# Kernel tuning notes

Hardware: AMD Instinct MI355X
Metric: run time of the kernel (lower is better)

## Reference

```python
import jax, jax.numpy as jnp
import numpy as np

L = 16            # clip_len
STRIDES = (2, 2)
RADII = (0.15, 0.3)
NSAMPLES = (16, 32)
EPS = 1e-5
NEG_SLOPE = 0.2


def _fps(xyz, npoint):
    # furthest point sampling, xyz: (N, 3) -> (npoint,) int32 indices, start at 0
    N = xyz.shape[0]
    def step(carry, _):
        mind, last = carry
        d = jnp.sum((xyz - xyz[last]) ** 2, axis=-1)
        mind = jnp.minimum(mind, d)
        nxt = jnp.argmax(mind).astype(jnp.int32)
        return (mind, nxt), nxt
    _, rest = jax.lax.scan(step, (jnp.full((N,), 1e10, xyz.dtype), jnp.int32(0)), None, length=npoint - 1)
    return jnp.concatenate([jnp.zeros((1,), jnp.int32), rest])


def _shift_point(xyz, batch, N):
    # torch.roll(points, -1, dims=1) over the temporal axis, with last-frame extrapolation fix
    p = xyz.reshape(batch // L, L, N, 3)
    s = jnp.roll(p, -1, axis=1)
    shift_mean = jnp.mean(s[:, :-1] - p[:, :-1], axis=1)   # (Bc, N, 3)
    s = s.at[:, -1].set(p[:, -1] + shift_mean)
    return s.reshape(batch, N, 3)


def _conv_bn_lrelu(x, w, g, b):
    # 1x1 Conv2d (no bias) + GroupBN (per-channel over all other dims) + LeakyReLU(0.2)
    y = jnp.einsum('oc,bcnk->bonk', w, x)
    mu = jnp.mean(y, axis=(0, 2, 3), keepdims=True)
    var = jnp.var(y, axis=(0, 2, 3), keepdims=True)
    y = (y - mu) * jax.lax.rsqrt(var + EPS) * g[None, :, None, None] + b[None, :, None, None]
    return jnp.where(y > 0, y, NEG_SLOPE * y)


def _sa_module(xyz, features, stride, radius, nsample, layers):
    # xyz: (B, N, 3), features: (B, C, N)
    batch, N = xyz.shape[0], xyz.shape[1]
    q = _shift_point(xyz, batch, N)
    npoint = N // stride if stride > 1 else N
    if stride > 1:
        idx = jax.vmap(lambda p: _fps(p, npoint))(jax.lax.stop_gradient(q))  # (B, npoint)
        q = jax.vmap(lambda p, ix: p[ix])(q, idx)                            # (B, npoint, 3)
    # ball query: first `nsample` neighbors of each query within `radius`, padded with first hit
    d2 = jnp.sum((q[:, :, None, :] - xyz[:, None, :, :]) ** 2, axis=-1)      # (B, npoint, N)
    mask = d2 < radius * radius
    cand = jnp.where(mask, jnp.arange(N, dtype=jnp.int32)[None, None, :], N)
    srt = jnp.sort(cand, axis=-1)[..., :nsample]
    first = srt[..., :1]
    gidx = jnp.where(srt == N, first, srt)
    gidx = jnp.where(gidx == N, 0, gidx)                                     # fallback: no neighbor
    grouped_xyz = jax.vmap(lambda pts, ix: pts[ix])(xyz, gidx)               # (B, npoint, ns, 3)
    dp = (grouped_xyz - q[:, :, None, :]) / radius                           # normalize_dp
    dist = jnp.linalg.norm(dp, axis=-1)                                      # (B, npoint, ns) -> 4th grouped channel
    feats = jnp.swapaxes(features, 1, 2)                                     # (B, N, C)
    grouped_f = jax.vmap(lambda f, ix: f[ix])(feats, gidx)                   # (B, npoint, ns, C)
    x = jnp.concatenate([dp, grouped_f], axis=-1)                            # (B, npoint, ns, 3 + C)
    x = jnp.transpose(x, (0, 3, 1, 2))                                       # (B, 3 + C, npoint, ns)
    for (w, g, b) in layers:
        x = _conv_bn_lrelu(x, w, g, b)
    gate = jax.nn.sigmoid(dist)[:, None, :, :]                               # sigmoid(points[:, -1:])
    out = jnp.max(gate * x, axis=-1)                                         # (B, Cout, npoint)
    return q, out


def _forward(xyz, w1a, g1a, b1a, w1b, g1b, b1b, w2a, g2a, b2a, w2b, g2b, b2b):
    features = jnp.swapaxes(xyz, 1, 2)                                       # features default = xyz^T
    q1, f1 = _sa_module(xyz, features, STRIDES[0], RADII[0], NSAMPLES[0],
                        [(w1a, g1a, b1a), (w1b, g1b, b1b)])
    q2, f2 = _sa_module(q1, f1, STRIDES[1], RADII[1], NSAMPLES[1],
                        [(w2a, g2a, b2a), (w2b, g2b, b2b)])
    return f2                                                                # (32, 256, 128)


def setup_inputs() -> dict:
    key = jax.random.key(0)
    ks = jax.random.split(key, 5)
    B, N = 32, 512   # B = 2 clips * clip_len 16
    xyz = jax.random.uniform(ks[0], (B, N, 3), jnp.float32)
    def w(k, o, i):
        return jax.random.normal(k, (o, i), jnp.float32) / np.sqrt(i).astype(np.float32)
    return {
        'xyz': xyz,
        'w1a': w(ks[1], 64, 6),    'g1a': jnp.ones(64),  'b1a': jnp.zeros(64),
        'w1b': w(ks[2], 128, 64),  'g1b': jnp.ones(128), 'b1b': jnp.zeros(128),
        'w2a': w(ks[3], 128, 131), 'g2a': jnp.ones(128), 'b2a': jnp.zeros(128),
        'w2b': w(ks[4], 256, 128), 'g2b': jnp.ones(256), 'b2b': jnp.zeros(256),
    }


def reference(xyz, w1a, g1a, b1a, w1b, g1b, b1b, w2a, g2a, b2a, w2b, g2b, b2b):
    return _forward(xyz, w1a, g1a, b1a, w1b, g1b, b1b, w2a, g2a, b2a, w2b, g2b, b2b)
```

## Files before the change

### kernel.cpp

```cpp
#include <hip/hip_runtime.h>
#include <hip/hip_bf16.h>
#include <math.h>


#define BATCH 32
#define MCOLS 131072
#define CGRID 2048

typedef __attribute__((ext_vector_type(8))) short short8;
typedef __attribute__((ext_vector_type(4))) short short4v;
typedef __attribute__((ext_vector_type(4))) float f32x4;

__device__ __forceinline__ float b2f(short s) {
    return __uint_as_float(((unsigned)(unsigned short)s) << 16);
}
__device__ __forceinline__ short f2b(float f) {
    __hip_bfloat16 h = __float2bfloat16(f);
    return (short)__builtin_bit_cast(unsigned short, h);
}
__device__ __forceinline__ float dpp_row16_sum(float v) {
    int x;
    x = __builtin_amdgcn_update_dpp(0, __float_as_int(v), 0x111, 0xf, 0xf, true);
    v += __int_as_float(x);
    x = __builtin_amdgcn_update_dpp(0, __float_as_int(v), 0x112, 0xf, 0xf, true);
    v += __int_as_float(x);
    x = __builtin_amdgcn_update_dpp(0, __float_as_int(v), 0x114, 0xf, 0xf, true);
    v += __int_as_float(x);
    x = __builtin_amdgcn_update_dpp(0, __float_as_int(v), 0x118, 0xf, 0xf, true);
    v += __int_as_float(x);
    return v;
}
template<int C>
__device__ __forceinline__ float dpp_max(float v) {
    int x = __builtin_amdgcn_update_dpp(0, __float_as_int(v), C, 0xf, 0xf, true);
    return fmaxf(v, __int_as_float(x));
}
__device__ __forceinline__ float readlane_f(float v, int lane) {
    return __int_as_float(__builtin_amdgcn_readlane(__float_as_int(v), lane));
}

__global__ void prep_w(const float* __restrict__ w, int O, int C, int CK,
                       short* __restrict__ hi, short* __restrict__ lo) {
    int t = blockIdx.x * 256 + threadIdx.x;
    if (t >= O * CK) return;
    int o = t / CK, c = t % CK;
    float f = (c < C) ? w[o * C + c] : 0.f;
    short h = f2b(f);
    float fh = b2f(h);
    int NT = O >> 4;
    int ot = o >> 4, l15 = o & 15;
    int kc = c >> 5, quad = (c & 31) >> 3, j = c & 7;
    size_t idx = (((size_t)kc * NT + ot) * 64 + quad * 16 + l15) * 8 + j;
    hi[idx] = h;
    lo[idx] = f2b(f - fh);
}

template<int N>
__global__ void shift_kernel(const float* __restrict__ xyz, float* __restrict__ qout) {
    int t = blockIdx.x * 256 + threadIdx.x;
    if (t >= BATCH * N * 3) return;
    int c = t % 3;
    int n = (t / 3) % N;
    int b = t / (3 * N);
    int l = b & 15;
    float v;
    if (l < 15) {
        v = xyz[((size_t)(b + 1) * N + n) * 3 + c];
    } else {
        int g0 = b - 15;
        float acc = 0.f;
        for (int i = 0; i < 15; ++i) {
            float d = __fsub_rn(xyz[((size_t)(g0 + i + 1) * N + n) * 3 + c],
                                xyz[((size_t)(g0 + i) * N + n) * 3 + c]);
            acc = __fadd_rn(acc, d);
        }
        v = __fadd_rn(xyz[((size_t)b * N + n) * 3 + c], __fdiv_rn(acc, 15.f));
    }
    qout[t] = v;
}

template<int N, int NPOINT>
__global__ __launch_bounds__(64) void fps_kernel(const float* __restrict__ q,
                                                 float* __restrict__ qsel) {
    int b = blockIdx.x;
    int lane = threadIdx.x;
    constexpr int P = N / 64;
    __shared__ float4 qp[N];
    __shared__ int sel[NPOINT];
    const float* qb = q + (size_t)b * N * 3;
    for (int j = lane; j < N; j += 64)
        qp[j] = make_float4(qb[j * 3 + 0], qb[j * 3 + 1], qb[j * 3 + 2], 0.f);
    if (lane == 0) sel[0] = 0;
    __syncthreads();
    float px[P], py[P], pz[P], mind[P];
#pragma unroll
    for (int p = 0; p < P; ++p) {
        float4 v = qp[lane * P + p];
        px[p] = v.x; py[p] = v.y; pz[p] = v.z;
        mind[p] = 1e10f;
    }
    float4 L0 = qp[0];
    float lx = L0.x, ly = L0.y, lz = L0.z;
    for (int s = 1; s < NPOINT; ++s) {
        float bestd = -1.f;
        int bestp = 0;
        float bx = 0.f, by = 0.f, bz = 0.f;
#pragma unroll
        for (int p = 0; p < P; ++p) {
            float dx = __fsub_rn(px[p], lx);
            float dy = __fsub_rn(py[p], ly);
            float dz = __fsub_rn(pz[p], lz);
            float d = __fadd_rn(__fadd_rn(__fmul_rn(dx, dx), __fmul_rn(dy, dy)),
                                __fmul_rn(dz, dz));
            float mn = fminf(mind[p], d);
            mind[p] = mn;
            bool g = mn > bestd;
            bestd = g ? mn : bestd;
            bestp = g ? p : bestp;
            bx = g ? px[p] : bx;
            by = g ? py[p] : by;
            bz = g ? pz[p] : bz;
        }
        float m = bestd;
        m = dpp_max<0x111>(m);
        m = dpp_max<0x112>(m);
        m = dpp_max<0x114>(m);
        m = dpp_max<0x118>(m);
        m = dpp_max<0x142>(m);
        m = dpp_max<0x143>(m);
        float maxd = readlane_f(m, 63);
        unsigned long long msk = __ballot(bestd == maxd);
        int winner = (int)__builtin_ctzll(msk);
        int wp = __builtin_amdgcn_readlane(bestp, winner);
        int last = winner * P + wp;
        lx = readlane_f(bx, winner);
        ly = readlane_f(by, winner);
        lz = readlane_f(bz, winner);
        if (lane == 0) sel[s] = last;
    }
    __syncthreads();
    for (int i = lane; i < NPOINT; i += 64) {
        float4 Pt = qp[sel[i]];
        size_t o = ((size_t)b * NPOINT + i) * 3;
        qsel[o + 0] = Pt.x;
        qsel[o + 1] = Pt.y;
        qsel[o + 2] = Pt.z;
    }
}

template<int N, int NPOINT, int NS, int CF, int CK>
__global__ __launch_bounds__(256) void ballq_kernel(
        const float* __restrict__ xyz,
        const float* __restrict__ qpts,
        const float* __restrict__ feats,
        float r2, float radius,
        short* __restrict__ X, float* __restrict__ gate) {
    static_assert((NS & (NS - 1)) == 0, "NS pow2");
    int lane = threadIdx.x & 63;
    int wib = threadIdx.x >> 6;
    int wid = blockIdx.x * 4 + wib;
    int b = wid / NPOINT;
    int i = wid % NPOINT;
    const float* qp = qpts + ((size_t)b * NPOINT + i) * 3;
    float qx = qp[0], qy = qp[1], qz = qp[2];
    __shared__ int gsh[4][NS];
    int* gidx = gsh[wib];
    int taken = 0, first = 0;
    bool any = false;
#pragma unroll
    for (int base = 0; base < N; base += 64) {
        int j = base + lane;
        const float* p = xyz + ((size_t)b * N + j) * 3;
        float dx = __fsub_rn(qx, p[0]);
        float dy = __fsub_rn(qy, p[1]);
        float dz = __fsub_rn(qz, p[2]);
        float d2 = __fadd_rn(__fadd_rn(__fmul_rn(dx, dx), __fmul_rn(dy, dy)),
                             __fmul_rn(dz, dz));
        bool in = d2 < r2;
        unsigned long long mk = __ballot(in);
        if (!any && mk) { first = base + __builtin_ctzll(mk); any = true; }
        int cb = __builtin_popcountll(mk & ((1ull << lane) - 1ull));
        int slot = taken + cb;
        if (in && slot < NS) gidx[slot] = j;
        taken += (int)__builtin_popcountll(mk);
    }
    if (taken < NS) {
        for (int s = taken + lane; s < NS; s += 64) gidx[s] = any ? first : 0;
    }
    __syncthreads();
    int m0 = (b * NPOINT + i) * NS;
    if (lane < NS) {
        int g = gidx[lane];
        const float* p = xyz + ((size_t)b * N + g) * 3;
        float dx = (p[0] - qx) / radius;
        float dy = (p[1] - qy) / radius;
        float dz = (p[2] - qz) / radius;
        float dist = sqrtf(dx * dx + dy * dy + dz * dz);
        gate[m0 + lane] = 1.f / (1.f + expf(-dist));
    }
    for (int e = lane; e < NS * CK; e += 64) {
        int s = e / CK;
        int c = e % CK;
        int g = gidx[s];
        float v;
        if (c < 3) {
            float qc = (c == 0) ? qx : ((c == 1) ? qy : qz);
            v = (xyz[((size_t)b * N + g) * 3 + c] - qc) / radius;
        } else if (c < 3 + CF) {
            v = feats[((size_t)b * N + g) * CF + (c - 3)];
        } else {
            v = 0.f;
        }
        X[(size_t)(m0 + s) * CK + c] = f2b(v);
    }
}

template<int CK, int O, bool AFF>
__global__ __launch_bounds__(256, 3) void mfma_conv(
        const short* __restrict__ X, const short* __restrict__ Whi,
        const short* __restrict__ Wlo, const float* __restrict__ ss,
        short* __restrict__ Y, float* __restrict__ pS, float* __restrict__ pS2) {
    constexpr int KC = CK / 32;
    constexpr int NT = O / 16;
    constexpr int OW = NT / 4;
    constexpr int LR = CK + 8;
    constexpr int CB = CK / 8;
    __shared__ __align__(16) short xs[64 * LR];
    __shared__ __align__(16) short wh[NT * 512];
    __shared__ __align__(16) short wl[NT * 512];
    __shared__ float ssl[AFF ? 2 * CK : 1];
    __shared__ float sblk[O], s2blk[O];
    int tid = threadIdx.x;
    int m0 = blockIdx.x * 64;

    if constexpr (AFF) {
        for (int i = tid; i < 2 * CK; i += 256) ssl[i] = ss[i];
        __syncthreads();
    }
    for (int idx = tid; idx < 64 * CB; idx += 256) {
        int r = idx / CB;
        int col = (idx % CB) * 8;
        short8 v = *(const short8*)(X + (size_t)(m0 + r) * CK + col);
        if constexpr (AFF) {
#pragma unroll
            for (int i = 0; i < 8; ++i) {
                float f = b2f(v[i]);
                f = fmaf(f, ssl[col + i], ssl[CK + col + i]);
                f = f > 0.f ? f : 0.2f * f;
                v[i] = f2b(f);
            }
        }
        *(short8*)(xs + r * LR + col) = v;
    }

    int lane = tid & 63;
    int wave = tid >> 6;
    int l15 = lane & 15;
    int quad = lane >> 4;
    int obase = wave * OW * 16;

    f32x4 acc[4][OW];
#pragma unroll
    for (int mt = 0; mt < 4; ++mt)
#pragma unroll
        for (int ot = 0; ot < OW; ++ot) acc[mt][ot] = (f32x4){0.f, 0.f, 0.f, 0.f};

    for (int kc = 0; kc < KC; ++kc) {
        __syncthreads();
        {
            const short8* gH = (const short8*)Whi + (size_t)kc * NT * 64;
            const short8* gL = (const short8*)Wlo + (size_t)kc * NT * 64;
            short8* lH = (short8*)wh;
            short8* lL = (short8*)wl;
            for (int i = tid; i < NT * 64; i += 256) { lH[i] = gH[i]; lL[i] = gL[i]; }
        }
        __syncthreads();
        short8 bf[4];
#pragma unroll
        for (int mt = 0; mt < 4; ++mt)
            bf[mt] = *(const short8*)(xs + (mt * 16 + l15) * LR + kc * 32 + quad * 8);
#pragma unroll
        for (int ot = 0; ot < OW; ++ot) {
            short8 ah = ((const short8*)wh)[(wave * OW + ot) * 64 + lane];
            short8 al = ((const short8*)wl)[(wave * OW + ot) * 64 + lane];
#pragma unroll
            for (int mt = 0; mt < 4; ++mt) {
                acc[mt][ot] = __builtin_amdgcn_mfma_f32_16x16x32_bf16(ah, bf[mt], acc[mt][ot], 0, 0, 0);
                acc[mt][ot] = __builtin_amdgcn_mfma_f32_16x16x32_bf16(al, bf[mt], acc[mt][ot], 0, 0, 0);
            }
        }
    }

#pragma unroll
    for (int mt = 0; mt < 4; ++mt) {
        size_t ybase = (size_t)(m0 + mt * 16 + l15) * O + obase + quad * 4;
#pragma unroll
        for (int ot = 0; ot < OW; ++ot) {
            short4v pk;
#pragma unroll
            for (int r4 = 0; r4 < 4; ++r4) pk[r4] = f2b(acc[mt][ot][r4]);
            *(short4v*)(Y + ybase + ot * 16) = pk;
        }
    }
#pragma unroll
    for (int ot = 0; ot < OW; ++ot) {
#pragma unroll
        for (int r4 = 0; r4 < 4; ++r4) {
            float s = 0.f, s2 = 0.f;
#pragma unroll
            for (int mt = 0; mt < 4; ++mt) {
                float v = acc[mt][ot][r4];
                s += v;
                s2 = fmaf(v, v, s2);
            }
            s = dpp_row16_sum(s);
            s2 = dpp_row16_sum(s2);
            if (l15 == 15) {
                int o = obase + ot * 16 + quad * 4 + r4;
                sblk[o] = s;
                s2blk[o] = s2;
            }
        }
    }
    __syncthreads();
    for (int o = tid; o < O; o += 256) {
        pS [(size_t)o * CGRID + blockIdx.x] = sblk[o];
        pS2[(size_t)o * CGRID + blockIdx.x] = s2blk[o];
    }
}

template<int O>
__global__ __launch_bounds__(256) void stats_fin(
        const float* __restrict__ pS, const float* __restrict__ pS2,
        const float* __restrict__ gm, const float* __restrict__ bt,
        float* __restrict__ norm) {
    int o = blockIdx.x;
    float s = 0.f, s2 = 0.f;
    for (int p = threadIdx.x; p < CGRID; p += 256) {
        s += pS[(size_t)o * CGRID + p];
        s2 += pS2[(size_t)o * CGRID + p];
    }
#pragma unroll
    for (int off = 32; off >= 1; off >>= 1) {
        s  += __shfl_xor(s,  off, 64);
        s2 += __shfl_xor(s2, off, 64);
    }
    __shared__ float sh[8];
    int wid = threadIdx.x >> 6;
    if ((threadIdx.x & 63) == 0) { sh[wid] = s; sh[4 + wid] = s2; }
    __syncthreads();
    if (threadIdx.x == 0) {
        float S  = sh[0] + sh[1] + sh[2] + sh[3];
        float S2 = sh[4] + sh[5] + sh[6] + sh[7];
        const float invM = 1.f / (float)MCOLS;
        float mu = S * invM;
        float var = S2 * invM - mu * mu;
        float sc = gm[o] * rsqrtf(var + 1e-5f);
        norm[o] = sc;
        norm[O + o] = bt[o] - mu * sc;
    }
}

template<int NS, int NPOINT, int O>
__global__ __launch_bounds__(256) void pool1_kernel(
        const short* __restrict__ Y, const float* __restrict__ norm,
        const float* __restrict__ gate, float* __restrict__ out) {
    int t = blockIdx.x * 256 + threadIdx.x;
    int o = t % O;
    int n = (t / O) % NPOINT;
    int b = t / (O * NPOINT);
    int m0 = (b * NPOINT + n) * NS;
    float sc = norm[o], sf = norm[O + o];
    float best = -INFINITY;
#pragma unroll
    for (int k = 0; k < NS; ++k) {
        float v = fmaf(b2f(Y[(size_t)(m0 + k) * O + o]), sc, sf);
        v = v > 0.f ? v : 0.2f * v;
        best = fmaxf(best, gate[m0 + k] * v);
    }
    out[t] = best;
}

__global__ __launch_bounds__(256) void pool2_kernel(
        const short* __restrict__ Y, const float* __restrict__ norm,
        const float* __restrict__ gate, float* __restrict__ out) {
    constexpr int NS = 32, NPOINT = 128, O = 256;
    int b  = blockIdx.x >> 3;
    int oc = (blockIdx.x >> 1) & 3;
    int nc = blockIdx.x & 1;
    __shared__ float trans[64][65];
    int tid = threadIdx.x;
    for (int w = 0; w < 16; ++w) {
        int idx = w * 256 + tid;
        int o_l = idx & 63;
        int n_l = idx >> 6;
        int o = oc * 64 + o_l;
        int n = nc * 64 + n_l;
        int m0 = (b * NPOINT + n) * NS;
        float sc = norm[o], sf = norm[O + o];
        float best = -INFINITY;
#pragma unroll
        for (int k = 0; k < NS; ++k) {
            float v = fmaf(b2f(Y[(size_t)(m0 + k) * O + o]), sc, sf);
            v = v > 0.f ? v : 0.2f * v;
            best = fmaxf(best, gate[m0 + k] * v);
        }
        trans[o_l][n_l] = best;
    }
    __syncthreads();
    for (int w = 0; w < 16; ++w) {
        int idx = w * 256 + tid;
        int o_l = idx >> 6;
        int n_l = idx & 63;
        out[((size_t)b * O + oc * 64 + o_l) * NPOINT + nc * 64 + n_l] = trans[o_l][n_l];
    }
}

extern "C" void kernel_launch(void* const* d_in, const int* in_sizes, int n_in,
                              void* d_out, int out_size, void* d_ws, size_t ws_size,
                              hipStream_t stream) {
    const float* xyz = (const float*)d_in[0];
    const float* w1a = (const float*)d_in[1];
    const float* g1a = (const float*)d_in[2];
    const float* b1a = (const float*)d_in[3];
    const float* w1b = (const float*)d_in[4];
    const float* g1b = (const float*)d_in[5];
    const float* b1b = (const float*)d_in[6];
    const float* w2a = (const float*)d_in[7];
    const float* g2a = (const float*)d_in[8];
    const float* b2a = (const float*)d_in[9];
    const float* w2b = (const float*)d_in[10];
    const float* g2b = (const float*)d_in[11];
    const float* b2b = (const float*)d_in[12];

    char* ws = (char*)d_ws;
    constexpr size_t OFF_Q1C   = 0;
    constexpr size_t OFF_GATE1 = 98304;
    constexpr size_t OFF_Q2C   = 622592;
    constexpr size_t OFF_GATE2 = 671744;
    constexpr size_t OFF_NORM  = 1196032;
    constexpr size_t OFF_W     = 1204224;
    constexpr size_t OFF_PS    = 1499136;
    constexpr size_t OFF_PS2   = 3596288;
    constexpr size_t OFF_A     = 5693440;
    constexpr size_t OFF_B     = 39247872;
    constexpr size_t OFF_F1    = OFF_B + 41943040;

    float* q1c   = (float*)(ws + OFF_Q1C);
    float* gate1 = (float*)(ws + OFF_GATE1);
    float* q2c   = (float*)(ws + OFF_Q2C);
    float* gate2 = (float*)(ws + OFF_GATE2);
    float* n1a   = (float*)(ws + OFF_NORM);
    float* n1b   = (float*)(ws + OFF_NORM + 512);
    float* n2a   = (float*)(ws + OFF_NORM + 1536);
    float* n2b   = (float*)(ws + OFF_NORM + 2560);
    short* w1aH  = (short*)(ws + OFF_W);
    short* w1aL  = w1aH + 2048;
    short* w1bH  = w1aL + 2048;
    short* w1bL  = w1bH + 8192;
    short* w2aH  = w1bL + 8192;
    short* w2aL  = w2aH + 20480;
    short* w2bH  = w2aL + 20480;
    short* w2bL  = w2bH + 32768;
    float* pS    = (float*)(ws + OFF_PS);
    float* pS2   = (float*)(ws + OFF_PS2);

    char* A = ws + OFF_A;
    char* B = ws + OFF_B;
    short* X1  = (short*)A;
    short* Y1a = (short*)B;
    short* Y1b = (short*)A;
    short* X2  = (short*)B;
    short* Y2a = (short*)A;
    short* Y2b = (short*)B;
    float* qs1 = (float*)B;
    float* qs2 = (float*)A;
    float* f1  = (float*)(ws + OFF_F1);

    const float r2_1 = (float)(0.15 * 0.15);
    const float r2_2 = (float)(0.3 * 0.3);

    prep_w<<<8,   256, 0, stream>>>(w1a, 64, 6, 32, w1aH, w1aL);
    prep_w<<<32,  256, 0, stream>>>(w1b, 128, 64, 64, w1bH, w1bL);
    prep_w<<<80,  256, 0, stream>>>(w2a, 128, 131, 160, w2aH, w2aL);
    prep_w<<<128, 256, 0, stream>>>(w2b, 256, 128, 128, w2bH, w2bL);

    shift_kernel<512><<<192, 256, 0, stream>>>(xyz, qs1);
    fps_kernel<512, 256><<<32, 64, 0, stream>>>(qs1, q1c);
    ballq_kernel<512, 256, 16, 3, 32><<<2048, 256, 0, stream>>>(
        xyz, q1c, xyz, r2_1, 0.15f, X1, gate1);
    mfma_conv<32, 64, false><<<CGRID, 256, 0, stream>>>(X1, w1aH, w1aL, nullptr, Y1a, pS, pS2);
    stats_fin<64><<<64, 256, 0, stream>>>(pS, pS2, g1a, b1a, n1a);
    mfma_conv<64, 128, true><<<CGRID, 256, 0, stream>>>(Y1a, w1bH, w1bL, n1a, Y1b, pS, pS2);
    stats_fin<128><<<128, 256, 0, stream>>>(pS, pS2, g1b, b1b, n1b);
    pool1_kernel<16, 256, 128><<<4096, 256, 0, stream>>>(Y1b, n1b, gate1, f1);

    shift_kernel<256><<<96, 256, 0, stream>>>(q1c, qs2);
    fps_kernel<256, 128><<<32, 64, 0, stream>>>(qs2, q2c);
    ballq_kernel<256, 128, 32, 128, 160><<<1024, 256, 0, stream>>>(
        q1c, q2c, f1, r2_2, 0.3f, X2, gate2);
    mfma_conv<160, 128, false><<<CGRID, 256, 0, stream>>>(X2, w2aH, w2aL, nullptr, Y2a, pS, pS2);
    stats_fin<128><<<128, 256, 0, stream>>>(pS, pS2, g2a, b2a, n2a);
    mfma_conv<128, 256, true><<<CGRID, 256, 0, stream>>>(Y2a, w2bH, w2bL, n2a, Y2b, pS, pS2);
    stats_fin<256><<<256, 256, 0, stream>>>(pS, pS2, g2b, b2b, n2b);
    pool2_kernel<<<256, 256, 0, stream>>>(Y2b, n2b, gate2, (float*)d_out);
}
```

Before: 409.5 us.

## Fuse temporal shift into FPS kernel and use tree-max selection in FPS loop

Removes the separate shift_kernel launches and computes the rolled/extrapolated coordinates while loading points into shared memory inside fps_kernel. The per-thread argmax in the FPS loop becomes a tree fmax reduction followed by an equality scan to recover index and coordinates, which shortens the serial dependency chain on each of the sequential FPS iterations. The goal is to save two launches and the round trip of the shifted coordinates through global memory, and to cut latency in the FPS loop that bounds this pipeline. The cost is that the block handling frame 15 now does the 15-frame mean loads itself, serially within one 64-thread block.

```diff
diff --git a/kernel.cpp b/kernel.cpp
--- a/kernel.cpp
+++ b/kernel.cpp
@@ -55,41 +55,36 @@
     lo[idx] = f2b(f - fh);
 }
 
-template<int N>
-__global__ void shift_kernel(const float* __restrict__ xyz, float* __restrict__ qout) {
-    int t = blockIdx.x * 256 + threadIdx.x;
-    if (t >= BATCH * N * 3) return;
-    int c = t % 3;
-    int n = (t / 3) % N;
-    int b = t / (3 * N);
-    int l = b & 15;
-    float v;
-    if (l < 15) {
-        v = xyz[((size_t)(b + 1) * N + n) * 3 + c];
-    } else {
-        int g0 = b - 15;
-        float acc = 0.f;
-        for (int i = 0; i < 15; ++i) {
-            float d = __fsub_rn(xyz[((size_t)(g0 + i + 1) * N + n) * 3 + c],
-                                xyz[((size_t)(g0 + i) * N + n) * 3 + c]);
-            acc = __fadd_rn(acc, d);
-        }
-        v = __fadd_rn(xyz[((size_t)b * N + n) * 3 + c], __fdiv_rn(acc, 15.f));
-    }
-    qout[t] = v;
-}
-
 template<int N, int NPOINT>
-__global__ __launch_bounds__(64) void fps_kernel(const float* __restrict__ q,
+__global__ __launch_bounds__(64) void fps_kernel(const float* __restrict__ src,
                                                  float* __restrict__ qsel) {
     int b = blockIdx.x;
     int lane = threadIdx.x;
+    int l = b & 15;
     constexpr int P = N / 64;
     __shared__ float4 qp[N];
     __shared__ int sel[NPOINT];
-    const float* qb = q + (size_t)b * N * 3;
-    for (int j = lane; j < N; j += 64)
-        qp[j] = make_float4(qb[j * 3 + 0], qb[j * 3 + 1], qb[j * 3 + 2], 0.f);
+    if (l < 15) {
+        const float* s = src + (size_t)(b + 1) * N * 3;
+        for (int j = lane; j < N; j += 64)
+            qp[j] = make_float4(s[j * 3 + 0], s[j * 3 + 1], s[j * 3 + 2], 0.f);
+    } else {
+        int g0 = b - 15;
+        for (int j = lane; j < N; j += 64) {
+            float v[3];
+#pragma unroll
+            for (int c = 0; c < 3; ++c) {
+                float acc = 0.f;
+                for (int i = 0; i < 15; ++i) {
+                    float d = __fsub_rn(src[((size_t)(g0 + i + 1) * N + j) * 3 + c],
+                                        src[((size_t)(g0 + i) * N + j) * 3 + c]);
+                    acc = __fadd_rn(acc, d);
+                }
+                v[c] = __fadd_rn(src[((size_t)b * N + j) * 3 + c], __fdiv_rn(acc, 15.f));
+            }
+            qp[j] = make_float4(v[0], v[1], v[2], 0.f);
+        }
+    }
     if (lane == 0) sel[0] = 0;
     __syncthreads();
     float px[P], py[P], pz[P], mind[P];
@@ -102,9 +97,7 @@
     float4 L0 = qp[0];
     float lx = L0.x, ly = L0.y, lz = L0.z;
     for (int s = 1; s < NPOINT; ++s) {
-        float bestd = -1.f;
-        int bestp = 0;
-        float bx = 0.f, by = 0.f, bz = 0.f;
+        float mn[P];
 #pragma unroll
         for (int p = 0; p < P; ++p) {
             float dx = __fsub_rn(px[p], lx);
@@ -112,16 +105,19 @@
             float dz = __fsub_rn(pz[p], lz);
             float d = __fadd_rn(__fadd_rn(__fmul_rn(dx, dx), __fmul_rn(dy, dy)),
                                 __fmul_rn(dz, dz));
-            float mn = fminf(mind[p], d);
-            mind[p] = mn;
-            bool g = mn > bestd;
-            bestd = g ? mn : bestd;
-            bestp = g ? p : bestp;
-            bx = g ? px[p] : bx;
-            by = g ? py[p] : by;
-            bz = g ? pz[p] : bz;
-        }
-        float m = bestd;
+            float m2 = fminf(mind[p], d);
+            mind[p] = m2;
+            mn[p] = m2;
+        }
+        float t[P];
+#pragma unroll
+        for (int p = 0; p < P; ++p) t[p] = mn[p];
+#pragma unroll
+        for (int w = P / 2; w >= 1; w >>= 1)
+#pragma unroll
+            for (int p = 0; p < w; ++p) t[p] = fmaxf(t[p], t[p + w]);
+        float local = t[0];
+        float m = local;
         m = dpp_max<0x111>(m);
         m = dpp_max<0x112>(m);
         m = dpp_max<0x114>(m);
@@ -129,10 +125,24 @@
         m = dpp_max<0x142>(m);
         m = dpp_max<0x143>(m);
         float maxd = readlane_f(m, 63);
-        unsigned long long msk = __ballot(bestd == maxd);
+        int enc = 0;
+        float bx = px[0], by = py[0], bz = pz[0];
+#pragma unroll
+        for (int p = P - 1; p >= 1; --p) {
+            bool e = (mn[p] == local);
+            enc = e ? p : enc;
+            bx = e ? px[p] : bx;
+            by = e ? py[p] : by;
+            bz = e ? pz[p] : bz;
+        }
+        bool e0 = (mn[0] == local);
+        enc = e0 ? 0 : enc;
+        bx = e0 ? px[0] : bx;
+        by = e0 ? py[0] : by;
+        bz = e0 ? pz[0] : bz;
+        unsigned long long msk = __ballot(local == maxd);
         int winner = (int)__builtin_ctzll(msk);
-        int wp = __builtin_amdgcn_readlane(bestp, winner);
-        int last = winner * P + wp;
+        int last = winner * P + __builtin_amdgcn_readlane(enc, winner);
         lx = readlane_f(bx, winner);
         ly = readlane_f(by, winner);
         lz = readlane_f(bz, winner);
@@ -473,8 +483,6 @@
     short* X2  = (short*)B;
     short* Y2a = (short*)A;
     short* Y2b = (short*)B;
-    float* qs1 = (float*)B;
-    float* qs2 = (float*)A;
     float* f1  = (float*)(ws + OFF_F1);
 
     const float r2_1 = (float)(0.15 * 0.15);
@@ -485,8 +493,7 @@
     prep_w<<<80,  256, 0, stream>>>(w2a, 128, 131, 160, w2aH, w2aL);
     prep_w<<<128, 256, 0, stream>>>(w2b, 256, 128, 128, w2bH, w2bL);
 
-    shift_kernel<512><<<192, 256, 0, stream>>>(xyz, qs1);
-    fps_kernel<512, 256><<<32, 64, 0, stream>>>(qs1, q1c);
+    fps_kernel<512, 256><<<32, 64, 0, stream>>>(xyz, q1c);
     ballq_kernel<512, 256, 16, 3, 32><<<2048, 256, 0, stream>>>(
         xyz, q1c, xyz, r2_1, 0.15f, X1, gate1);
     mfma_conv<32, 64, false><<<CGRID, 256, 0, stream>>>(X1, w1aH, w1aL, nullptr, Y1a, pS, pS2);
@@ -495,8 +502,7 @@
     stats_fin<128><<<128, 256, 0, stream>>>(pS, pS2, g1b, b1b, n1b);
     pool1_kernel<16, 256, 128><<<4096, 256, 0, stream>>>(Y1b, n1b, gate1, f1);
 
-    shift_kernel<256><<<96, 256, 0, stream>>>(q1c, qs2);
-    fps_kernel<256, 128><<<32, 64, 0, stream>>>(qs2, q2c);
+    fps_kernel<256, 128><<<32, 64, 0, stream>>>(q1c, q2c);
     ballq_kernel<256, 128, 32, 128, 160><<<1024, 256, 0, stream>>>(
         q1c, q2c, f1, r2_2, 0.3f, X2, gate2);
     mfma_conv<160, 128, false><<<CGRID, 256, 0, stream>>>(X2, w2aH, w2aL, nullptr, Y2a, pS, pS2);
```

Result: slower. 434.3 us (+6.0%).

## Split furthest point sampling across four waves per batch

Applied to the files above, without the earlier changes.

The FPS kernel now runs 256 threads (four wavefronts) per batch instead of one wavefront, so each thread holds a quarter as many points. Each step does a per-wave DPP max reduction and ballot, then a cross-wave reduction through double-buffered shared memory with one __syncthreads per step. This cuts per-thread serial work in the latency-bound sequential FPS loop, but adds a block barrier and LDS round trip to every one of the hundreds of steps. Tie-breaking is kept to the lowest index, matching argmax.

```diff
diff --git a/kernel.cpp b/kernel.cpp
--- a/kernel.cpp
+++ b/kernel.cpp
@@ -80,31 +80,33 @@
 }
 
 template<int N, int NPOINT>
-__global__ __launch_bounds__(64) void fps_kernel(const float* __restrict__ q,
-                                                 float* __restrict__ qsel) {
+__global__ __launch_bounds__(256) void fps_kernel(const float* __restrict__ q,
+                                                  float* __restrict__ qsel) {
     int b = blockIdx.x;
-    int lane = threadIdx.x;
-    constexpr int P = N / 64;
+    int tid = threadIdx.x;
+    int lane = tid & 63;
+    int wave = tid >> 6;
+    constexpr int P = N / 256;
     __shared__ float4 qp[N];
     __shared__ int sel[NPOINT];
+    __shared__ float cd[2][4], cx[2][4], cy[2][4], cz[2][4];
+    __shared__ int ci[2][4];
     const float* qb = q + (size_t)b * N * 3;
-    for (int j = lane; j < N; j += 64)
+    for (int j = tid; j < N; j += 256)
         qp[j] = make_float4(qb[j * 3 + 0], qb[j * 3 + 1], qb[j * 3 + 2], 0.f);
-    if (lane == 0) sel[0] = 0;
+    if (tid == 0) sel[0] = 0;
     __syncthreads();
     float px[P], py[P], pz[P], mind[P];
 #pragma unroll
     for (int p = 0; p < P; ++p) {
-        float4 v = qp[lane * P + p];
+        float4 v = qp[tid * P + p];
         px[p] = v.x; py[p] = v.y; pz[p] = v.z;
         mind[p] = 1e10f;
     }
     float4 L0 = qp[0];
     float lx = L0.x, ly = L0.y, lz = L0.z;
     for (int s = 1; s < NPOINT; ++s) {
-        float bestd = -1.f;
-        int bestp = 0;
-        float bx = 0.f, by = 0.f, bz = 0.f;
+        float mn[P];
 #pragma unroll
         for (int p = 0; p < P; ++p) {
             float dx = __fsub_rn(px[p], lx);
@@ -112,34 +114,64 @@
             float dz = __fsub_rn(pz[p], lz);
             float d = __fadd_rn(__fadd_rn(__fmul_rn(dx, dx), __fmul_rn(dy, dy)),
                                 __fmul_rn(dz, dz));
-            float mn = fminf(mind[p], d);
-            mind[p] = mn;
-            bool g = mn > bestd;
-            bestd = g ? mn : bestd;
-            bestp = g ? p : bestp;
-            bx = g ? px[p] : bx;
-            by = g ? py[p] : by;
-            bz = g ? pz[p] : bz;
-        }
-        float m = bestd;
+            float m2 = fminf(mind[p], d);
+            mind[p] = m2;
+            mn[p] = m2;
+        }
+        float local = mn[0];
+#pragma unroll
+        for (int p = 1; p < P; ++p) local = fmaxf(local, mn[p]);
+        float m = local;
         m = dpp_max<0x111>(m);
         m = dpp_max<0x112>(m);
         m = dpp_max<0x114>(m);
         m = dpp_max<0x118>(m);
         m = dpp_max<0x142>(m);
         m = dpp_max<0x143>(m);
-        float maxd = readlane_f(m, 63);
-        unsigned long long msk = __ballot(bestd == maxd);
-        int winner = (int)__builtin_ctzll(msk);
-        int wp = __builtin_amdgcn_readlane(bestp, winner);
-        int last = winner * P + wp;
-        lx = readlane_f(bx, winner);
-        ly = readlane_f(by, winner);
-        lz = readlane_f(bz, winner);
-        if (lane == 0) sel[s] = last;
+        float wmax = readlane_f(m, 63);
+        unsigned long long msk = __ballot(local == wmax);
+        int wl = (int)__builtin_ctzll(msk);
+        int enc = P - 1;
+        float bx = px[P - 1], by = py[P - 1], bz = pz[P - 1];
+#pragma unroll
+        for (int p = P - 2; p >= 0; --p) {
+            bool e = (mn[p] == local);
+            enc = e ? p : enc;
+            bx = e ? px[p] : bx;
+            by = e ? py[p] : by;
+            bz = e ? pz[p] : bz;
+        }
+        float wx = readlane_f(bx, wl);
+        float wy = readlane_f(by, wl);
+        float wz = readlane_f(bz, wl);
+        int   wj = (wave * 64 + wl) * P + __builtin_amdgcn_readlane(enc, wl);
+        int sl = s & 1;
+        if (lane == 0) {
+            cd[sl][wave] = wmax;
+            cx[sl][wave] = wx;
+            cy[sl][wave] = wy;
+            cz[sl][wave] = wz;
+            ci[sl][wave] = wj;
+        }
+        __syncthreads();
+        float d0 = cd[sl][0], d1 = cd[sl][1], d2 = cd[sl][2], d3 = cd[sl][3];
+        float g = fmaxf(fmaxf(d0, d1), fmaxf(d2, d3));
+        float nx = cx[sl][3], ny = cy[sl][3], nz = cz[sl][3];
+        int nj = ci[sl][3];
+        bool e2 = (d2 == g);
+        nx = e2 ? cx[sl][2] : nx; ny = e2 ? cy[sl][2] : ny;
+        nz = e2 ? cz[sl][2] : nz; nj = e2 ? ci[sl][2] : nj;
+        bool e1 = (d1 == g);
+        nx = e1 ? cx[sl][1] : nx; ny = e1 ? cy[sl][1] : ny;
+        nz = e1 ? cz[sl][1] : nz; nj = e1 ? ci[sl][1] : nj;
+        bool e0 = (d0 == g);
+        nx = e0 ? cx[sl][0] : nx; ny = e0 ? cy[sl][0] : ny;
+        nz = e0 ? cz[sl][0] : nz; nj = e0 ? ci[sl][0] : nj;
+        lx = nx; ly = ny; lz = nz;
+        if (tid == 0) sel[s] = nj;
     }
     __syncthreads();
-    for (int i = lane; i < NPOINT; i += 64) {
+    for (int i = tid; i < NPOINT; i += 256) {
         float4 Pt = qp[sel[i]];
         size_t o = ((size_t)b * NPOINT + i) * 3;
         qsel[o + 0] = Pt.x;
@@ -486,7 +518,7 @@
     prep_w<<<128, 256, 0, stream>>>(w2b, 256, 128, 128, w2bH, w2bL);
 
     shift_kernel<512><<<192, 256, 0, stream>>>(xyz, qs1);
-    fps_kernel<512, 256><<<32, 64, 0, stream>>>(qs1, q1c);
+    fps_kernel<512, 256><<<32, 256, 0, stream>>>(qs1, q1c);
     ballq_kernel<512, 256, 16, 3, 32><<<2048, 256, 0, stream>>>(
         xyz, q1c, xyz, r2_1, 0.15f, X1, gate1);
     mfma_conv<32, 64, false><<<CGRID, 256, 0, stream>>>(X1, w1aH, w1aL, nullptr, Y1a, pS, pS2);
@@ -496,7 +528,7 @@
     pool1_kernel<16, 256, 128><<<4096, 256, 0, stream>>>(Y1b, n1b, gate1, f1);
 
     shift_kernel<256><<<96, 256, 0, stream>>>(q1c, qs2);
-    fps_kernel<256, 128><<<32, 64, 0, stream>>>(qs2, q2c);
+    fps_kernel<256, 128><<<32, 256, 0, stream>>>(qs2, q2c);
     ballq_kernel<256, 128, 32, 128, 160><<<1024, 256, 0, stream>>>(
         q1c, q2c, f1, r2_2, 0.3f, X2, gate2);
     mfma_conv<160, 128, false><<<CGRID, 256, 0, stream>>>(X2, w2aH, w2aL, nullptr, Y2a, pS, pS2);
```

Result: slower. 498.9 us (+21.8%).
